# Optimization experiments

Hardware: AMD Instinct MI355X
Metric: run time of the kernel (lower is better)

## Reference

```python
import jax, jax.numpy as jnp
import numpy as np

B, D, H, NC = 4096, 128, 4, 10
HD = D // H
EPS = 1e-5


def _ln(x, g, b):
    m = jnp.mean(x, axis=-1, keepdims=True)
    v = jnp.var(x, axis=-1, keepdims=True)
    return (x - m) * jax.lax.rsqrt(v + EPS) * g + b


def _mlp(x, w1, b1, w2, b2):
    h = jax.nn.gelu(x @ w1.T + b1, approximate=False)  # nn.GELU default = exact erf
    return h @ w2.T + b2


def setup_inputs():
    key = jax.random.key(0)
    ks = iter(jax.random.split(key, 40))
    w = lambda *s: jax.random.normal(next(ks), s, dtype=jnp.float32) * 0.02
    inp = {
        'coords': jax.random.uniform(next(ks), (B, 2), dtype=jnp.float32),
        'labels': jax.random.randint(next(ks), (B,), 0, NC),
        'ce_w': w(D, 2), 'ce_b': w(D),
        'emb': w(NC, D),
        'sa_in_w': w(3 * D, D), 'sa_in_b': w(3 * D),
        'sa_out_w': w(D, D), 'sa_out_b': w(D),
        'n1_g': jnp.ones(D), 'n1_b': jnp.zeros(D),
        'm1_w1': w(4 * D, D), 'm1_b1': w(4 * D), 'm1_w2': w(D, 4 * D), 'm1_b2': w(D),
        'n2_g': jnp.ones(D), 'n2_b': jnp.zeros(D),
        'ca_in_w': w(3 * D, D), 'ca_in_b': w(3 * D),
        'ca_out_w': w(D, D), 'ca_out_b': w(D),
        'n3_g': jnp.ones(D), 'n3_b': jnp.zeros(D),
        'm2_w1': w(4 * D, D), 'm2_b1': w(4 * D), 'm2_w2': w(D, 4 * D), 'm2_b2': w(D),
        'n4_g': jnp.ones(D), 'n4_b': jnp.zeros(D),
        'fin_w': w(1, D), 'fin_b': w(1),
    }
    return inp


def reference(coords, labels, ce_w, ce_b, emb, sa_in_w, sa_in_b, sa_out_w, sa_out_b,
              n1_g, n1_b, m1_w1, m1_b1, m1_w2, m1_b2, n2_g, n2_b,
              ca_in_w, ca_in_b, ca_out_w, ca_out_b, n3_g, n3_b,
              m2_w1, m2_b1, m2_w2, m2_b2, n4_g, n4_b, fin_w, fin_b):
    # --- vectorized positional encoding (original loops over batch) ---
    div = 10000.0 ** (2.0 * jnp.arange(D // 2, dtype=jnp.float32) / D)  # [D/2]
    pe_sin = jnp.sin(coords[:, 0:1] / div)  # even slots
    pe_cos = jnp.cos(coords[:, 1:2] / div)  # odd slots
    pe = jnp.stack([pe_sin, pe_cos], axis=-1).reshape(B, D)

    x = coords @ ce_w.T + ce_b + pe  # [B, D]

    # --- self-attention: seq_len = B, batch = 1 (torch seq-first semantics) ---
    qkv = x @ sa_in_w.T + sa_in_b  # [B, 3D]
    q, k, v = jnp.split(qkv, 3, axis=-1)
    q = q.reshape(B, H, HD); k = k.reshape(B, H, HD); v = v.reshape(B, H, HD)
    scores = jnp.einsum('qhd,khd->hqk', q, k) / jnp.sqrt(jnp.float32(HD))  # [H,B,B]
    attn = jax.nn.softmax(scores, axis=-1)
    sa = jnp.einsum('hqk,khd->qhd', attn, v).reshape(B, D) @ sa_out_w.T + sa_out_b

    x = _ln(x + sa, n1_g, n1_b)
    x = _ln(x + _mlp(x, m1_w1, m1_b1, m1_w2, m1_b2), n2_g, n2_b)

    # --- cross-attention: per-sample q_len = kv_len = 1 -> softmax over a
    # single key is exactly 1, so output = out_proj(v_proj(label_emb)) ---
    lab = emb[labels]  # [B, D]
    wv = ca_in_w[2 * D:]; bv = ca_in_b[2 * D:]
    ca = (lab @ wv.T + bv) @ ca_out_w.T + ca_out_b

    x = _ln(x + ca, n3_g, n3_b)
    x = _ln(x + _mlp(x, m2_w1, m2_b1, m2_w2, m2_b2), n4_g, n4_b)

    return jax.nn.sigmoid(x @ fin_w.T + fin_b)  # [B, 1]
```

## Files before the change

### kernel.cpp

```cpp
#include <hip/hip_runtime.h>
#include <hip/hip_bf16.h>


typedef __bf16 bf16_t;
typedef __bf16 bf16x8 __attribute__((ext_vector_type(8)));
typedef __bf16 bf16x4 __attribute__((ext_vector_type(4)));
typedef float  f32x4  __attribute__((ext_vector_type(4)));

__device__ __forceinline__ f32x4 mfma16(bf16x8 a, bf16x8 b, f32x4 c) {
  return __builtin_amdgcn_mfma_f32_16x16x32_bf16(a, b, c, 0, 0, 0);
}

__global__ __launch_bounds__(512) void k_init(const float* __restrict__ coords,
                                              const float* __restrict__ ce_w,
                                              const float* __restrict__ ce_b,
                                              float* __restrict__ xf,
                                              bf16_t* __restrict__ xb,
                                              const float* __restrict__ s0,
                                              const float* __restrict__ s1,
                                              const float* __restrict__ s2,
                                              const float* __restrict__ s3,
                                              const float* __restrict__ s4,
                                              const float* __restrict__ s5,
                                              bf16_t* __restrict__ wdst,
                                              const float* __restrict__ emb,
                                              const float* __restrict__ wvp,
                                              const float* __restrict__ bvp,
                                              const float* __restrict__ cow,
                                              const float* __restrict__ cob,
                                              float* __restrict__ tab) {
  __shared__ float embs[10][128];
  __shared__ float t1[10][128];
  const int bid = blockIdx.x;
  const int tid = threadIdx.x;
  if (bid < 256) {
    int c = bid * 512 + tid;
    int row = c >> 5, d0 = (c & 31) * 4;
    float c0 = coords[row * 2 + 0];
    float c1 = coords[row * 2 + 1];
    f32x4 xv; bf16x4 xo;
#pragma unroll
    for (int r = 0; r < 4; r++) {
      int d = d0 + r, j = d >> 1;
      float inv = exp2f(-0.20762050593045953f * (float)j);
      float pe  = (d & 1) ? cosf(c1 * inv) : sinf(c0 * inv);
      float x = c0 * ce_w[2 * d] + c1 * ce_w[2 * d + 1] + ce_b[d] + pe;
      xv[r] = x; xo[r] = (bf16_t)x;
    }
    *(f32x4*)(xf + (size_t)row * 128 + d0) = xv;
    *(bf16x4*)(xb + (size_t)row * 128 + d0) = xo;

    if (c < 81920) {
      const float* src; int off;
      if      (c < 12288) { src = s0; off = c; }
      else if (c < 16384) { src = s1; off = c - 12288; }
      else if (c < 32768) { src = s2; off = c - 16384; }
      else if (c < 49152) { src = s3; off = c - 32768; }
      else if (c < 65536) { src = s4; off = c - 49152; }
      else                { src = s5; off = c - 65536; }
      f32x4 v = *(const f32x4*)(src + (size_t)off * 4);
      bf16x4 o = {(bf16_t)v[0], (bf16_t)v[1], (bf16_t)v[2], (bf16_t)v[3]};
      *(bf16x4*)(wdst + (size_t)c * 4) = o;
    }
  } else {
    for (int i = tid; i < 1280; i += 512) embs[i >> 7][i & 127] = emb[i];
    __syncthreads();
    for (int o = tid; o < 1280; o += 512) {
      int cc = o >> 7, n = o & 127;
      float acc = bvp[n];
      const float* wr = wvp + n * 128;
      for (int k2 = 0; k2 < 128; k2++) acc += embs[cc][k2] * wr[k2];
      t1[cc][n] = acc;
    }
    __syncthreads();
    for (int o = tid; o < 1280; o += 512) {
      int cc = o >> 7, dd = o & 127;
      float acc = cob[dd];
      const float* wr = cow + dd * 128;
      for (int n = 0; n < 128; n++) acc += t1[cc][n] * wr[n];
      tab[o] = acc;
    }
  }
}

__global__ __launch_bounds__(256) void k_gemm_qkv(const bf16_t* __restrict__ X,
                                                  const bf16_t* __restrict__ Wb,
                                                  const float* __restrict__ bias,
                                                  bf16_t* __restrict__ outB,
                                                  bf16_t* __restrict__ vTout) {
  const int tid  = threadIdx.x;
  const int lane = tid & 63;
  const int wv   = tid >> 6;
  const int l15  = lane & 15;
  const int quad = lane >> 4;
  const int xbase = blockIdx.x * 64 + (wv >> 1) * 32;
  const int wbase = blockIdx.y * 64 + (wv & 1) * 32;

  const bf16_t* wr0 = Wb + (size_t)(wbase + l15) * 128 + quad * 8;
  const bf16_t* xr0 = X  + (size_t)(xbase + l15) * 128 + quad * 8;

  f32x4 acc[2][2];
  const f32x4 zero4 = {0.f, 0.f, 0.f, 0.f};
  for (int i = 0; i < 2; i++)
    for (int t = 0; t < 2; t++) acc[i][t] = zero4;

#pragma unroll
  for (int kk = 0; kk < 128; kk += 32) {
    bf16x8 a0 = *(const bf16x8*)(wr0 + kk);
    bf16x8 a1 = *(const bf16x8*)(wr0 + 16 * 128 + kk);
    bf16x8 b0 = *(const bf16x8*)(xr0 + kk);
    bf16x8 b1 = *(const bf16x8*)(xr0 + 16 * 128 + kk);
    acc[0][0] = mfma16(a0, b0, acc[0][0]);
    acc[0][1] = mfma16(a0, b1, acc[0][1]);
    acc[1][0] = mfma16(a1, b0, acc[1][0]);
    acc[1][1] = mfma16(a1, b1, acc[1][1]);
  }

  f32x4 bv[2];
  bv[0] = *(const f32x4*)(bias + wbase + quad * 4);
  bv[1] = *(const f32x4*)(bias + wbase + 16 + quad * 4);
#pragma unroll
  for (int t = 0; t < 2; t++) {
    int row = xbase + t * 16 + l15;
#pragma unroll
    for (int i = 0; i < 2; i++) {
      int col0 = wbase + i * 16 + quad * 4;
      f32x4 v = acc[i][t] + bv[i];
      bf16x4 o = {(bf16_t)v[0], (bf16_t)v[1], (bf16_t)v[2], (bf16_t)v[3]};
      *(bf16x4*)(outB + (size_t)row * 384 + col0) = o;
      if (col0 >= 256) {
#pragma unroll
        for (int r = 0; r < 4; r++)
          vTout[(size_t)(col0 - 256 + r) * 4096 + row] = (bf16_t)v[r];
      }
    }
  }
}

__global__ __launch_bounds__(256, 4) void k_attn(const bf16_t* __restrict__ qkv,
                                                 const bf16_t* __restrict__ vT,
                                                 bf16_t* __restrict__ opart,
                                                 float* __restrict__ lpart) {
  __shared__ bf16_t kbuf[128][36];
  __shared__ bf16_t vbuf[32][136];
  __shared__ bf16_t pt[4][2][16][72];

  const int tid  = threadIdx.x;
  const int lane = tid & 63;
  const int wv   = tid >> 6;
  const int l15  = lane & 15;
  const int quad = lane >> 4;
  const int blk  = blockIdx.x;
  const int h    = blk & 3;
  const int ks   = (blk >> 2) & 7;
  const int qt   = (blk >> 5) * 4 + wv;
  const int q0   = qt * 32;
  const int kb   = ks * 512;
  const int task = (qt * 8 + ks) * 4 + h;

  bf16x8 qfA, qfB;
  {
    bf16x8 ra = *(const bf16x8*)(qkv + (size_t)(q0 + l15) * 384 + h * 32 + quad * 8);
    bf16x8 rb = *(const bf16x8*)(qkv + (size_t)(q0 + 16 + l15) * 384 + h * 32 + quad * 8);
#pragma unroll
    for (int j = 0; j < 8; j++) {
      qfA[j] = (bf16_t)((float)ra[j] * 0.17677669529663687f);
      qfB[j] = (bf16_t)((float)rb[j] * 0.17677669529663687f);
    }
  }

  const f32x4 zero4 = {0.f, 0.f, 0.f, 0.f};
  f32x4 oA0 = zero4, oA1 = zero4, oB0 = zero4, oB1 = zero4;
  float laccA = 0.f, laccB = 0.f;

  for (int kk = 0; kk < 512; kk += 128) {
    __syncthreads();
#pragma unroll
    for (int rep = 0; rep < 2; rep++) {
      int idx = rep * 256 + tid;
      int row = idx >> 2, seg = idx & 3;
      bf16x8 t8 = *(const bf16x8*)(qkv + (size_t)(kb + kk + row) * 384
                                   + 128 + h * 32 + seg * 8);
      *(bf16x8*)&kbuf[row][seg * 8] = t8;
      int dim = idx >> 4, vseg = idx & 15;
      bf16x8 v8 = *(const bf16x8*)(vT + (size_t)(h * 32 + dim) * 4096
                                   + kb + kk + vseg * 8);
      *(bf16x8*)&vbuf[dim][vseg * 8] = v8;
    }
    __syncthreads();

#pragma unroll
    for (int half = 0; half < 2; half++) {
      const int ko = half * 64;
      bf16x8 kf0 = *(const bf16x8*)&kbuf[ko + l15][quad * 8];
      bf16x8 kf1 = *(const bf16x8*)&kbuf[ko + 16 + l15][quad * 8];
      bf16x8 kf2 = *(const bf16x8*)&kbuf[ko + 32 + l15][quad * 8];
      bf16x8 kf3 = *(const bf16x8*)&kbuf[ko + 48 + l15][quad * 8];

      f32x4 sA[4], sB[4];
      sA[0] = mfma16(kf0, qfA, zero4);
      sA[1] = mfma16(kf1, qfA, zero4);
      sA[2] = mfma16(kf2, qfA, zero4);
      sA[3] = mfma16(kf3, qfA, zero4);
      sB[0] = mfma16(kf0, qfB, zero4);
      sB[1] = mfma16(kf1, qfB, zero4);
      sB[2] = mfma16(kf2, qfB, zero4);
      sB[3] = mfma16(kf3, qfB, zero4);

#pragma unroll
      for (int t = 0; t < 4; t++) {
        float a0 = __expf(sA[t][0]), a1 = __expf(sA[t][1]);
        float a2 = __expf(sA[t][2]), a3 = __expf(sA[t][3]);
        laccA += (a0 + a1) + (a2 + a3);
        bf16x4 pa = {(bf16_t)a0, (bf16_t)a1, (bf16_t)a2, (bf16_t)a3};
        *(bf16x4*)&pt[wv][0][l15][t * 16 + quad * 4] = pa;
        float b0 = __expf(sB[t][0]), b1 = __expf(sB[t][1]);
        float b2 = __expf(sB[t][2]), b3 = __expf(sB[t][3]);
        laccB += (b0 + b1) + (b2 + b3);
        bf16x4 pb = {(bf16_t)b0, (bf16_t)b1, (bf16_t)b2, (bf16_t)b3};
        *(bf16x4*)&pt[wv][1][l15][t * 16 + quad * 4] = pb;
      }

      bf16x8 pA0 = *(const bf16x8*)&pt[wv][0][l15][quad * 8];
      bf16x8 pA1 = *(const bf16x8*)&pt[wv][0][l15][32 + quad * 8];
      bf16x8 pB0 = *(const bf16x8*)&pt[wv][1][l15][quad * 8];
      bf16x8 pB1 = *(const bf16x8*)&pt[wv][1][l15][32 + quad * 8];

      bf16x8 v00 = *(const bf16x8*)&vbuf[l15][ko + quad * 8];
      bf16x8 v01 = *(const bf16x8*)&vbuf[16 + l15][ko + quad * 8];
      bf16x8 v10 = *(const bf16x8*)&vbuf[l15][ko + 32 + quad * 8];
      bf16x8 v11 = *(const bf16x8*)&vbuf[16 + l15][ko + 32 + quad * 8];

      oA0 = mfma16(pA0, v00, oA0);
      oA0 = mfma16(pA1, v10, oA0);
      oA1 = mfma16(pA0, v01, oA1);
      oA1 = mfma16(pA1, v11, oA1);
      oB0 = mfma16(pB0, v00, oB0);
      oB0 = mfma16(pB1, v10, oB0);
      oB1 = mfma16(pB0, v01, oB1);
      oB1 = mfma16(pB1, v11, oB1);
    }
  }

  laccA += __shfl_xor(laccA, 16, 64); laccA += __shfl_xor(laccA, 32, 64);
  laccB += __shfl_xor(laccB, 16, 64); laccB += __shfl_xor(laccB, 32, 64);
  if (quad == 0) {
    lpart[task * 32 + l15]      = laccA;
    lpart[task * 32 + 16 + l15] = laccB;
  }

  size_t ob = (size_t)task * 1024;
#pragma unroll
  for (int r = 0; r < 4; r++) {
    int qa = quad * 4 + r;
    opart[ob + qa * 32 + l15]             = (bf16_t)oA0[r];
    opart[ob + qa * 32 + 16 + l15]        = (bf16_t)oA1[r];
    opart[ob + (16 + qa) * 32 + l15]      = (bf16_t)oB0[r];
    opart[ob + (16 + qa) * 32 + 16 + l15] = (bf16_t)oB1[r];
  }
}

__global__ __launch_bounds__(512) void k_tail(
    const bf16_t* __restrict__ opart, const float* __restrict__ lpart,
    const float* __restrict__ xf,
    const bf16_t* __restrict__ wso, const float* __restrict__ bso,
    const float* __restrict__ n1g, const float* __restrict__ n1b,
    const bf16_t* __restrict__ w11, const float* __restrict__ b11,
    const bf16_t* __restrict__ w12, const float* __restrict__ b12,
    const float* __restrict__ n2g, const float* __restrict__ n2b,
    const int* __restrict__ labels, const float* __restrict__ tab,
    const float* __restrict__ n3g, const float* __restrict__ n3b,
    const bf16_t* __restrict__ w21, const float* __restrict__ b21,
    const bf16_t* __restrict__ w22, const float* __restrict__ b22,
    const float* __restrict__ n4g, const float* __restrict__ n4b,
    const float* __restrict__ fw, const float* __restrict__ fb,
    float* __restrict__ out) {
  __shared__ float  xs[16][132];
  __shared__ bf16_t xsb[16][136];
  __shared__ bf16_t att[16][136];
  __shared__ bf16_t hb[16][520];
  __shared__ float  red[2][16][8];
  __shared__ float  Ls[16][4];

  const int b    = blockIdx.x;
  const int tid  = threadIdx.x;
  const int lane = tid & 63;
  const int wv   = tid >> 6;
  const int l15  = lane & 15;
  const int quad = lane >> 4;
  const int row  = b * 16 + l15;
  const int cb1  = wv * 16;
  const int c1   = cb1 + quad * 4;
  const int cb4  = wv * 64;

  const f32x4 zero4 = {0.f, 0.f, 0.f, 0.f};

  if (tid < 64) {
    int rr = tid >> 2, hh = tid & 3;
    int q = b * 16 + rr, qt = q >> 5, ql = q & 31;
    float L = 0.f;
#pragma unroll
    for (int ks = 0; ks < 8; ks++) L += lpart[((qt * 8 + ks) * 4 + hh) * 32 + ql];
    Ls[rr][hh] = L;
  }
  __syncthreads();
#pragma unroll
  for (int r = 0; r < 4; r++) {
    int idx = r * 512 + tid;
    int rr = idx >> 7, d = idx & 127, hh = d >> 5, dd = d & 31;
    int q = b * 16 + rr, qt = q >> 5, ql = q & 31;
    float O = 0.f;
#pragma unroll
    for (int ks = 0; ks < 8; ks++)
      O += (float)opart[(size_t)((qt * 8 + ks) * 4 + hh) * 1024 + ql * 32 + dd];
    att[rr][d] = (bf16_t)(O / Ls[rr][hh]);
  }
  __syncthreads();

  {
    f32x4 acc = zero4;
    const bf16_t* ar = wso + (size_t)(cb1 + l15) * 128 + quad * 8;
#pragma unroll
    for (int kk = 0; kk < 128; kk += 32) {
      bf16x8 bfr = *(const bf16x8*)&att[l15][kk + quad * 8];
      acc = mfma16(*(const bf16x8*)(ar + kk), bfr, acc);
    }
    f32x4 v = acc + *(const f32x4*)(bso + c1)
                  + *(const f32x4*)(xf + (size_t)row * 128 + c1);
    float s  = (v[0] + v[1]) + (v[2] + v[3]);
    float sq = (v[0]*v[0] + v[1]*v[1]) + (v[2]*v[2] + v[3]*v[3]);
    s  += __shfl_xor(s, 16, 64);  s  += __shfl_xor(s, 32, 64);
    sq += __shfl_xor(sq, 16, 64); sq += __shfl_xor(sq, 32, 64);
    if (quad == 0) { red[0][l15][wv] = s; red[1][l15][wv] = sq; }
    __syncthreads();
    float S = 0.f, SQ = 0.f;
#pragma unroll
    for (int w2 = 0; w2 < 8; w2++) { S += red[0][l15][w2]; SQ += red[1][l15][w2]; }
    float mean = S * (1.f / 128.f);
    float rstd = rsqrtf(SQ * (1.f / 128.f) - mean * mean + 1e-5f);
    f32x4 y = (v - mean) * rstd * (*(const f32x4*)(n1g + c1))
            + *(const f32x4*)(n1b + c1);
    *(f32x4*)&xs[l15][c1] = y;
    bf16x4 o = {(bf16_t)y[0], (bf16_t)y[1], (bf16_t)y[2], (bf16_t)y[3]};
    *(bf16x4*)&xsb[l15][c1] = o;
  }
  __syncthreads();

  {
    f32x4 au[4] = {zero4, zero4, zero4, zero4};
#pragma unroll
    for (int kk = 0; kk < 128; kk += 32) {
      bf16x8 bfr = *(const bf16x8*)&xsb[l15][kk + quad * 8];
#pragma unroll
      for (int i = 0; i < 4; i++) {
        bf16x8 a = *(const bf16x8*)(w11 + (size_t)(cb4 + i * 16 + l15) * 128
                                    + kk + quad * 8);
        au[i] = mfma16(a, bfr, au[i]);
      }
    }
#pragma unroll
    for (int i = 0; i < 4; i++) {
      int c = cb4 + i * 16 + quad * 4;
      f32x4 vv = au[i] + *(const f32x4*)(b11 + c);
#pragma unroll
      for (int r = 0; r < 4; r++)
        vv[r] = 0.5f * vv[r] * (1.0f + erff(vv[r] * 0.70710678118654752f));
      bf16x4 o = {(bf16_t)vv[0], (bf16_t)vv[1], (bf16_t)vv[2], (bf16_t)vv[3]};
      *(bf16x4*)&hb[l15][c] = o;
    }
  }
  __syncthreads();

  {
    f32x4 acc = zero4;
    const bf16_t* ar = w12 + (size_t)(cb1 + l15) * 512 + quad * 8;
#pragma unroll 4
    for (int kk = 0; kk < 512; kk += 32) {
      bf16x8 bfr = *(const bf16x8*)&hb[l15][kk + quad * 8];
      acc = mfma16(*(const bf16x8*)(ar + kk), bfr, acc);
    }
    f32x4 v = acc + *(const f32x4*)(b12 + c1) + *(const f32x4*)&xs[l15][c1];
    float s  = (v[0] + v[1]) + (v[2] + v[3]);
    float sq = (v[0]*v[0] + v[1]*v[1]) + (v[2]*v[2] + v[3]*v[3]);
    s  += __shfl_xor(s, 16, 64);  s  += __shfl_xor(s, 32, 64);
    sq += __shfl_xor(sq, 16, 64); sq += __shfl_xor(sq, 32, 64);
    if (quad == 0) { red[0][l15][wv] = s; red[1][l15][wv] = sq; }
    __syncthreads();
    float S = 0.f, SQ = 0.f;
#pragma unroll
    for (int w2 = 0; w2 < 8; w2++) { S += red[0][l15][w2]; SQ += red[1][l15][w2]; }
    float mean = S * (1.f / 128.f);
    float rstd = rsqrtf(SQ * (1.f / 128.f) - mean * mean + 1e-5f);
    int lab = labels[row];
    f32x4 y = (v - mean) * rstd * (*(const f32x4*)(n2g + c1))
            + *(const f32x4*)(n2b + c1)
            + *(const f32x4*)(tab + (size_t)lab * 128 + c1);
    float s3  = (y[0] + y[1]) + (y[2] + y[3]);
    float sq3 = (y[0]*y[0] + y[1]*y[1]) + (y[2]*y[2] + y[3]*y[3]);
    s3  += __shfl_xor(s3, 16, 64);  s3  += __shfl_xor(s3, 32, 64);
    sq3 += __shfl_xor(sq3, 16, 64); sq3 += __shfl_xor(sq3, 32, 64);
    __syncthreads();
    if (quad == 0) { red[0][l15][wv] = s3; red[1][l15][wv] = sq3; }
    __syncthreads();
    float S3 = 0.f, SQ3 = 0.f;
#pragma unroll
    for (int w2 = 0; w2 < 8; w2++) { S3 += red[0][l15][w2]; SQ3 += red[1][l15][w2]; }
    float mean3 = S3 * (1.f / 128.f);
    float rstd3 = rsqrtf(SQ3 * (1.f / 128.f) - mean3 * mean3 + 1e-5f);
    f32x4 y3 = (y - mean3) * rstd3 * (*(const f32x4*)(n3g + c1))
             + *(const f32x4*)(n3b + c1);
    *(f32x4*)&xs[l15][c1] = y3;
    bf16x4 o = {(bf16_t)y3[0], (bf16_t)y3[1], (bf16_t)y3[2], (bf16_t)y3[3]};
    *(bf16x4*)&xsb[l15][c1] = o;
  }
  __syncthreads();

  {
    f32x4 au[4] = {zero4, zero4, zero4, zero4};
#pragma unroll
    for (int kk = 0; kk < 128; kk += 32) {
      bf16x8 bfr = *(const bf16x8*)&xsb[l15][kk + quad * 8];
#pragma unroll
      for (int i = 0; i < 4; i++) {
        bf16x8 a = *(const bf16x8*)(w21 + (size_t)(cb4 + i * 16 + l15) * 128
                                    + kk + quad * 8);
        au[i] = mfma16(a, bfr, au[i]);
      }
    }
#pragma unroll
    for (int i = 0; i < 4; i++) {
      int c = cb4 + i * 16 + quad * 4;
      f32x4 vv = au[i] + *(const f32x4*)(b21 + c);
#pragma unroll
      for (int r = 0; r < 4; r++)
        vv[r] = 0.5f * vv[r] * (1.0f + erff(vv[r] * 0.70710678118654752f));
      bf16x4 o = {(bf16_t)vv[0], (bf16_t)vv[1], (bf16_t)vv[2], (bf16_t)vv[3]};
      *(bf16x4*)&hb[l15][c] = o;
    }
  }
  __syncthreads();

  {
    f32x4 acc = zero4;
    const bf16_t* ar = w22 + (size_t)(cb1 + l15) * 512 + quad * 8;
#pragma unroll 4
    for (int kk = 0; kk < 512; kk += 32) {
      bf16x8 bfr = *(const bf16x8*)&hb[l15][kk + quad * 8];
      acc = mfma16(*(const bf16x8*)(ar + kk), bfr, acc);
    }
    f32x4 v = acc + *(const f32x4*)(b22 + c1) + *(const f32x4*)&xs[l15][c1];
    float s  = (v[0] + v[1]) + (v[2] + v[3]);
    float sq = (v[0]*v[0] + v[1]*v[1]) + (v[2]*v[2] + v[3]*v[3]);
    s  += __shfl_xor(s, 16, 64);  s  += __shfl_xor(s, 32, 64);
    sq += __shfl_xor(sq, 16, 64); sq += __shfl_xor(sq, 32, 64);
    if (quad == 0) { red[0][l15][wv] = s; red[1][l15][wv] = sq; }
    __syncthreads();
    float S = 0.f, SQ = 0.f;
#pragma unroll
    for (int w2 = 0; w2 < 8; w2++) { S += red[0][l15][w2]; SQ += red[1][l15][w2]; }
    float mean = S * (1.f / 128.f);
    float rstd = rsqrtf(SQ * (1.f / 128.f) - mean * mean + 1e-5f);
    f32x4 y = (v - mean) * rstd * (*(const f32x4*)(n4g + c1))
            + *(const f32x4*)(n4b + c1);
    f32x4 fwv = *(const f32x4*)(fw + c1);
    float dot = (y[0]*fwv[0] + y[1]*fwv[1]) + (y[2]*fwv[2] + y[3]*fwv[3]);
    dot += __shfl_xor(dot, 16, 64); dot += __shfl_xor(dot, 32, 64);
    __syncthreads();
    if (quad == 0) red[0][l15][wv] = dot;
    __syncthreads();
    if (wv == 0 && quad == 0) {
      float logit = fb[0];
#pragma unroll
      for (int w2 = 0; w2 < 8; w2++) logit += red[0][l15][w2];
      out[row] = 1.0f / (1.0f + expf(-logit));
    }
  }
}

extern "C" void kernel_launch(void* const* d_in, const int* in_sizes, int n_in,
                              void* d_out, int out_size, void* d_ws, size_t ws_size,
                              hipStream_t stream) {
  const float* coords  = (const float*)d_in[0];
  const int*   labels  = (const int*)d_in[1];
  const float* ce_w    = (const float*)d_in[2];
  const float* ce_b    = (const float*)d_in[3];
  const float* emb     = (const float*)d_in[4];
  const float* sa_in_w = (const float*)d_in[5];
  const float* sa_in_b = (const float*)d_in[6];
  const float* sa_out_w= (const float*)d_in[7];
  const float* sa_out_b= (const float*)d_in[8];
  const float* n1_g    = (const float*)d_in[9];
  const float* n1_b    = (const float*)d_in[10];
  const float* m1_w1   = (const float*)d_in[11];
  const float* m1_b1   = (const float*)d_in[12];
  const float* m1_w2   = (const float*)d_in[13];
  const float* m1_b2   = (const float*)d_in[14];
  const float* n2_g    = (const float*)d_in[15];
  const float* n2_b    = (const float*)d_in[16];
  const float* ca_in_w = (const float*)d_in[17];
  const float* ca_in_b = (const float*)d_in[18];
  const float* ca_out_w= (const float*)d_in[19];
  const float* ca_out_b= (const float*)d_in[20];
  const float* n3_g    = (const float*)d_in[21];
  const float* n3_b    = (const float*)d_in[22];
  const float* m2_w1   = (const float*)d_in[23];
  const float* m2_b1   = (const float*)d_in[24];
  const float* m2_w2   = (const float*)d_in[25];
  const float* m2_b2   = (const float*)d_in[26];
  const float* n4_g    = (const float*)d_in[27];
  const float* n4_b    = (const float*)d_in[28];
  const float* fin_w   = (const float*)d_in[29];
  const float* fin_b   = (const float*)d_in[30];
  float* outp = (float*)d_out;

  char* w = (char*)d_ws;
  float*  xf    = (float*)(w);
  float*  tab   = (float*)(w + 2097152);
  bf16_t* wsb   = (bf16_t*)(w + 2105344);
  bf16_t* xb    = (bf16_t*)(w + 2760704);
  bf16_t* qkvb  = (bf16_t*)(w + 4857856);
  bf16_t* vT    = (bf16_t*)(w + 8003584);
  bf16_t* opart = (bf16_t*)(w + 9052160);
  float*  lpart = (float*)(w + 17440768);

  bf16_t* w_sain  = wsb;
  bf16_t* w_saout = wsb + 49152;
  bf16_t* w_m1w1  = wsb + 65536;
  bf16_t* w_m1w2  = wsb + 131072;
  bf16_t* w_m2w1  = wsb + 196608;
  bf16_t* w_m2w2  = wsb + 262144;

  k_init<<<257, 512, 0, stream>>>(coords, ce_w, ce_b, xf, xb,
                                  sa_in_w, sa_out_w, m1_w1, m1_w2, m2_w1, m2_w2,
                                  wsb, emb, ca_in_w + 256 * 128, ca_in_b + 256,
                                  ca_out_w, ca_out_b, tab);
  k_gemm_qkv<<<dim3(64, 6), 256, 0, stream>>>(xb, w_sain, sa_in_b, qkvb, vT);
  k_attn<<<1024, 256, 0, stream>>>(qkvb, vT, opart, lpart);
  k_tail<<<256, 512, 0, stream>>>(opart, lpart, xf,
                                  w_saout, sa_out_b, n1_g, n1_b,
                                  w_m1w1, m1_b1, w_m1w2, m1_b2, n2_g, n2_b,
                                  labels, tab, n3_g, n3_b,
                                  w_m2w1, m2_b1, w_m2w2, m2_b2, n4_g, n4_b,
                                  fin_w, fin_b, outp);

  (void)in_sizes; (void)n_in; (void)out_size; (void)ws_size;
}
```

Baseline: 187.3 us.

## Drop global V-transpose buffer, transpose V into LDS inside attention kernel

The QKV GEMM no longer writes a separate transposed V buffer with scattered 2-byte stores. The attention kernel instead loads V rows straight from the QKV output and scatters them into the transposed shared-memory tile, which adds LDS bank conflicts during staging. The partial-output reduction in the tail kernel now uses 8-wide vector loads and a reciprocal multiply, and the positional encoding uses fast __sinf/__cosf intrinsics with lower accuracy.

```diff
diff --git a/kernel.cpp b/kernel.cpp
--- a/kernel.cpp
+++ b/kernel.cpp
@@ -43,7 +43,7 @@
     for (int r = 0; r < 4; r++) {
       int d = d0 + r, j = d >> 1;
       float inv = exp2f(-0.20762050593045953f * (float)j);
-      float pe  = (d & 1) ? cosf(c1 * inv) : sinf(c0 * inv);
+      float pe  = (d & 1) ? __cosf(c1 * inv) : __sinf(c0 * inv);
       float x = c0 * ce_w[2 * d] + c1 * ce_w[2 * d + 1] + ce_b[d] + pe;
       xv[r] = x; xo[r] = (bf16_t)x;
     }
@@ -86,8 +86,7 @@
 __global__ __launch_bounds__(256) void k_gemm_qkv(const bf16_t* __restrict__ X,
                                                   const bf16_t* __restrict__ Wb,
                                                   const float* __restrict__ bias,
-                                                  bf16_t* __restrict__ outB,
-                                                  bf16_t* __restrict__ vTout) {
+                                                  bf16_t* __restrict__ outB) {
   const int tid  = threadIdx.x;
   const int lane = tid & 63;
   const int wv   = tid >> 6;
@@ -128,17 +127,11 @@
       f32x4 v = acc[i][t] + bv[i];
       bf16x4 o = {(bf16_t)v[0], (bf16_t)v[1], (bf16_t)v[2], (bf16_t)v[3]};
       *(bf16x4*)(outB + (size_t)row * 384 + col0) = o;
-      if (col0 >= 256) {
-#pragma unroll
-        for (int r = 0; r < 4; r++)
-          vTout[(size_t)(col0 - 256 + r) * 4096 + row] = (bf16_t)v[r];
-      }
     }
   }
 }
 
 __global__ __launch_bounds__(256, 4) void k_attn(const bf16_t* __restrict__ qkv,
-                                                 const bf16_t* __restrict__ vT,
                                                  bf16_t* __restrict__ opart,
                                                  float* __restrict__ lpart) {
   __shared__ bf16_t kbuf[128][36];
@@ -182,10 +175,10 @@
       bf16x8 t8 = *(const bf16x8*)(qkv + (size_t)(kb + kk + row) * 384
                                    + 128 + h * 32 + seg * 8);
       *(bf16x8*)&kbuf[row][seg * 8] = t8;
-      int dim = idx >> 4, vseg = idx & 15;
-      bf16x8 v8 = *(const bf16x8*)(vT + (size_t)(h * 32 + dim) * 4096
-                                   + kb + kk + vseg * 8);
-      *(bf16x8*)&vbuf[dim][vseg * 8] = v8;
+      bf16x8 v8 = *(const bf16x8*)(qkv + (size_t)(kb + kk + row) * 384
+                                   + 256 + h * 32 + seg * 8);
+#pragma unroll
+      for (int j = 0; j < 8; j++) vbuf[seg * 8 + j][row] = v8[j];
     }
     __syncthreads();
 
@@ -304,16 +297,22 @@
     Ls[rr][hh] = L;
   }
   __syncthreads();
-#pragma unroll
-  for (int r = 0; r < 4; r++) {
-    int idx = r * 512 + tid;
-    int rr = idx >> 7, d = idx & 127, hh = d >> 5, dd = d & 31;
+  if (tid < 256) {
+    int oct = tid & 3, rr = (tid >> 2) & 15, hh = tid >> 6;
     int q = b * 16 + rr, qt = q >> 5, ql = q & 31;
-    float O = 0.f;
-#pragma unroll
-    for (int ks = 0; ks < 8; ks++)
-      O += (float)opart[(size_t)((qt * 8 + ks) * 4 + hh) * 1024 + ql * 32 + dd];
-    att[rr][d] = (bf16_t)(O / Ls[rr][hh]);
+    float acc[8] = {0.f, 0.f, 0.f, 0.f, 0.f, 0.f, 0.f, 0.f};
+#pragma unroll
+    for (int ks = 0; ks < 8; ks++) {
+      bf16x8 v = *(const bf16x8*)&opart[(size_t)((qt * 8 + ks) * 4 + hh) * 1024
+                                        + ql * 32 + oct * 8];
+#pragma unroll
+      for (int j = 0; j < 8; j++) acc[j] += (float)v[j];
+    }
+    float invL = 1.0f / Ls[rr][hh];
+    bf16x8 o;
+#pragma unroll
+    for (int j = 0; j < 8; j++) o[j] = (bf16_t)(acc[j] * invL);
+    *(bf16x8*)&att[rr][hh * 32 + oct * 8] = o;
   }
   __syncthreads();
 
@@ -519,7 +518,6 @@
   bf16_t* wsb   = (bf16_t*)(w + 2105344);
   bf16_t* xb    = (bf16_t*)(w + 2760704);
   bf16_t* qkvb  = (bf16_t*)(w + 4857856);
-  bf16_t* vT    = (bf16_t*)(w + 8003584);
   bf16_t* opart = (bf16_t*)(w + 9052160);
   float*  lpart = (float*)(w + 17440768);
 
@@ -534,8 +532,8 @@
                                   sa_in_w, sa_out_w, m1_w1, m1_w2, m2_w1, m2_w2,
                                   wsb, emb, ca_in_w + 256 * 128, ca_in_b + 256,
                                   ca_out_w, ca_out_b, tab);
-  k_gemm_qkv<<<dim3(64, 6), 256, 0, stream>>>(xb, w_sain, sa_in_b, qkvb, vT);
-  k_attn<<<1024, 256, 0, stream>>>(qkvb, vT, opart, lpart);
+  k_gemm_qkv<<<dim3(64, 6), 256, 0, stream>>>(xb, w_sain, sa_in_b, qkvb);
+  k_attn<<<1024, 256, 0, stream>>>(qkvb, opart, lpart);
   k_tail<<<256, 512, 0, stream>>>(opart, lpart, xf,
                                   w_saout, sa_out_b, n1_g, n1_b,
                                   w_m1w1, m1_b1, w_m1w2, m1_b2, n2_g, n2_b,
```

Result: no change. 190.4 us (+1.7%).
